# Optimization experiments

Measured on AMD Instinct MI355X. Metric: run time of the kernel, lower is better.

## Reference

```python
import jax, jax.numpy as jnp
import numpy as np

H = 300          # dim_hidden
L = 5            # num_layer
ATOM_VOCAB = 119
BOND_VOCAB = 5

def _bn(h, g, b):
    # train-mode BatchNorm1d over the leading (node/graph) dim
    m = h.mean(axis=0)
    v = h.var(axis=0)
    return g * (h - m) * jax.lax.rsqrt(v + 1e-5) + b

def setup_inputs() -> dict:
    key = jax.random.key(0)
    ks = jax.random.split(key, 24)
    N, E, B = 100000, 200000, 4096
    s = 0.02
    inp = {
        "x": jax.random.randint(ks[0], (N,), 0, ATOM_VOCAB),
        "edge_index": jax.random.randint(ks[1], (2, E), 0, N),
        "edge_attr": jax.random.randint(ks[2], (E,), 0, BOND_VOCAB),
        "batch": jnp.sort(jax.random.randint(ks[3], (N,), 0, B)),
        "batch_size": B,
        "atom_emb": jax.random.normal(ks[4], (ATOM_VOCAB, H)) * s,
        "bond_emb": jax.random.normal(ks[5], (BOND_VOCAB, H)) * s,
        "vn_emb": jax.random.normal(ks[6], (1, H)) * s,
        # per-layer GINE MLP: Linear(H,2H) -> ReLU -> Linear(2H,H), then BN
        "W1": jax.random.normal(ks[7], (L, H, 2 * H)) * s,
        "b1": jnp.zeros((L, 2 * H)),
        "W2": jax.random.normal(ks[8], (L, 2 * H, H)) * s,
        "b2": jnp.zeros((L, H)),
        "bn_g": jnp.ones((L, H)),
        "bn_b": jnp.zeros((L, H)),
        # virtual-node MLP: Lin(H,2H)-BN-ReLU-Lin(2H,H)-BN-ReLU
        "vW1": jax.random.normal(ks[9], (H, 2 * H)) * s,
        "vb1": jnp.zeros((2 * H,)),
        "vg1": jnp.ones((2 * H,)),
        "vbb1": jnp.zeros((2 * H,)),
        "vW2": jax.random.normal(ks[10], (2 * H, H)) * s,
        "vb2": jnp.zeros((H,)),
        "vg2": jnp.ones((H,)),
        "vbb2": jnp.zeros((H,)),
    }
    return inp

def reference(x, edge_index, edge_attr, batch, batch_size,
              atom_emb, bond_emb, vn_emb,
              W1, b1, W2, b2, bn_g, bn_b,
              vW1, vb1, vg1, vbb1, vW2, vb2, vg2, vbb2):
    N = x.shape[0]
    src, dst = edge_index[0], edge_index[1]
    h = atom_emb[x]                       # atom_encoder  [N,H]
    edge_feat = bond_emb[edge_attr]       # bond_encoder  [E,H]
    vn = jnp.broadcast_to(vn_emb[0], (batch_size, H))  # virtual node feats [B,H]
    for i in range(L):
        h_in = h + vn[batch]                                   # broadcast virtual node
        msg = jax.nn.relu(h_in[src] + edge_feat)               # GINE message  [E,H]
        aggr = jax.ops.segment_sum(msg, dst, num_segments=N)   # scatter-add
        pre = h_in + aggr                                      # eps = 0
        out = jax.nn.relu(pre @ W1[i] + b1[i]) @ W2[i] + b2[i]
        out = _bn(out, bn_g[i], bn_b[i])
        if i < L - 1:
            h = jax.nn.relu(out)
            pooled = jax.ops.segment_sum(h, batch, num_segments=batch_size) + vn
            t = jax.nn.relu(_bn(pooled @ vW1 + vb1, vg1, vbb1))
            vn = jax.nn.relu(_bn(t @ vW2 + vb2, vg2, vbb2))
        else:
            h = out                                            # no ReLU on last layer
    # readout: global add pool over graphs
    return jax.ops.segment_sum(h, batch, num_segments=batch_size)  # [B,H]
```

## Files before the change

### kernel.cpp

```cpp
#include <hip/hip_runtime.h>
#include <hip/hip_bf16.h>


#define HD 300
#define HD2 600
#define HDP 304
#define NLAYER 5
#define KS1 10
#define KS2 19
#define CT1P 40
#define CT2P 20
#define CAP 8
#define OVF_MAX 8192

typedef __attribute__((ext_vector_type(8))) short short8v;
typedef __attribute__((ext_vector_type(4))) short short4v;
typedef __attribute__((ext_vector_type(4))) float f32x4;

__device__ __forceinline__ short f2bf(float x) {
  union { float f; unsigned u; } v; v.f = x;
  unsigned r = v.u + 0x7fffu + ((v.u >> 16) & 1u);
  return (short)(r >> 16);
}
__device__ __forceinline__ float bf2f(short h) {
  union { unsigned u; float f; } v; v.u = ((unsigned)(unsigned short)h) << 16;
  return v.f;
}

__device__ __forceinline__ void cvt8(f32x4 x0, f32x4 x1, short8v& fh, short8v& fl) {
#pragma unroll
  for (int j = 0; j < 4; ++j) { short hi = f2bf(x0[j]); fh[j] = hi; fl[j] = f2bf(x0[j] - bf2f(hi)); }
#pragma unroll
  for (int j = 0; j < 4; ++j) { short hi = f2bf(x1[j]); fh[4 + j] = hi; fl[4 + j] = f2bf(x1[j] - bf2f(hi)); }
}

__global__ __launch_bounds__(256) void k_prep_wf(const float* __restrict__ W,
                                                 short* __restrict__ Whi,
                                                 short* __restrict__ Wlo,
                                                 int K, int C, int nks, int total) {
  int idx = blockIdx.x * 256 + threadIdx.x;
  if (idx >= total) return;
  int j = idx & 7, lane = (idx >> 3) & 63, t = idx >> 9;
  int ks = t % nks, ct = t / nks;
  int k = ks * 32 + (lane >> 4) * 8 + j;
  int c = ct * 16 + (lane & 15);
  float w = (k < K && c < C) ? W[(size_t)k * C + c] : 0.f;
  short hi = f2bf(w);
  Whi[idx] = hi;
  Wlo[idx] = f2bf(w - bf2f(hi));
}

__global__ __launch_bounds__(256, 3) void k_mlp_mfma(
    const unsigned short* __restrict__ ph, const unsigned short* __restrict__ pl,
    const short* __restrict__ W1hi, const short* __restrict__ W1lo,
    const float* __restrict__ b1,
    const short* __restrict__ W2hi, const short* __restrict__ W2lo,
    const float* __restrict__ b2, float* __restrict__ out,
    float* __restrict__ stats, int N) {
  __shared__ __align__(16) short hidh[32 * 320];
  __shared__ __align__(16) short hidl[32 * 320];
  char* hbh = (char*)hidh;
  char* hbl = (char*)hidl;
  const int tid = threadIdx.x;
  const int lane = tid & 63, cq = tid >> 6;
  const int li = lane & 15, g = lane >> 4;
  const int row0 = blockIdx.x * 32;
  const size_t r0b = (size_t)(row0 + li) * HDP;
  const size_t r1b = (size_t)(row0 + 16 + li) * HDP;

  f32x4 acc2[2][5];
#pragma unroll
  for (int rt = 0; rt < 2; ++rt)
#pragma unroll
    for (int t = 0; t < 5; ++t) acc2[rt][t] = (f32x4){0.f, 0.f, 0.f, 0.f};

#pragma unroll 1
  for (int hf = 0; hf < 2; ++hf) {
    const int ct0 = hf * 20 + cq * 5;
    f32x4 acc1[2][5];
#pragma unroll
    for (int rt = 0; rt < 2; ++rt)
#pragma unroll
      for (int t = 0; t < 5; ++t) acc1[rt][t] = (f32x4){0.f, 0.f, 0.f, 0.f};
    for (int ks = 0; ks < KS1; ++ks) {
      int k0 = ks * 32 + g * 8;
      short8v a0h = *(const short8v*)(ph + r0b + k0);
      short8v a0l = *(const short8v*)(pl + r0b + k0);
      short8v a1h = *(const short8v*)(ph + r1b + k0);
      short8v a1l = *(const short8v*)(pl + r1b + k0);
      const short8v* whp = (const short8v*)W1hi + ((size_t)ct0 * KS1 + ks) * 64 + lane;
      const short8v* wlp = (const short8v*)W1lo + ((size_t)ct0 * KS1 + ks) * 64 + lane;
#pragma unroll
      for (int ct = 0; ct < 5; ++ct) {
        short8v wh = whp[(size_t)ct * KS1 * 64];
        short8v wl = wlp[(size_t)ct * KS1 * 64];
        acc1[0][ct] = __builtin_amdgcn_mfma_f32_16x16x32_bf16(wh, a0h, acc1[0][ct], 0, 0, 0);
        acc1[0][ct] = __builtin_amdgcn_mfma_f32_16x16x32_bf16(wh, a0l, acc1[0][ct], 0, 0, 0);
        acc1[0][ct] = __builtin_amdgcn_mfma_f32_16x16x32_bf16(wl, a0h, acc1[0][ct], 0, 0, 0);
        acc1[1][ct] = __builtin_amdgcn_mfma_f32_16x16x32_bf16(wh, a1h, acc1[1][ct], 0, 0, 0);
        acc1[1][ct] = __builtin_amdgcn_mfma_f32_16x16x32_bf16(wh, a1l, acc1[1][ct], 0, 0, 0);
        acc1[1][ct] = __builtin_amdgcn_mfma_f32_16x16x32_bf16(wl, a1h, acc1[1][ct], 0, 0, 0);
      }
    }
    if (hf) __syncthreads();
#pragma unroll
    for (int ct = 0; ct < 5; ++ct) {
      int ctile = ct0 + ct, cc = ctile - hf * 20;
      float bb[4];
#pragma unroll
      for (int q = 0; q < 4; ++q) {
        int c = ctile * 16 + g * 4 + q;
        bb[q] = (c < HD2) ? b1[c] : 0.f;
      }
#pragma unroll
      for (int rt = 0; rt < 2; ++rt) {
        short4v vh, vl;
#pragma unroll
        for (int q = 0; q < 4; ++q) {
          float v = fmaxf(acc1[rt][ct][q] + bb[q], 0.f);
          short hi = f2bf(v);
          vh[q] = hi;
          vl[q] = f2bf(v - bf2f(hi));
        }
        int row = rt * 16 + li;
        int lin = row * 640 + cc * 32 + g * 8;
        int sw = (row & 7) << 4;
        *(short4v*)(hbh + (lin ^ sw)) = vh;
        *(short4v*)(hbl + (lin ^ sw)) = vl;
      }
    }
    __syncthreads();
    const int nks2 = hf ? 9 : 10;
    for (int ksl = 0; ksl < nks2; ++ksl) {
      int ksg = hf * 10 + ksl;
      int lin0 = li * 640 + ksl * 64 + g * 16;
      int sw0 = (li & 7) << 4;
      int lin1 = (16 + li) * 640 + ksl * 64 + g * 16;
      int sw1 = ((16 + li) & 7) << 4;
      short8v hh0 = *(const short8v*)(hbh + (lin0 ^ sw0));
      short8v hl0 = *(const short8v*)(hbl + (lin0 ^ sw0));
      short8v hh1 = *(const short8v*)(hbh + (lin1 ^ sw1));
      short8v hl1 = *(const short8v*)(hbl + (lin1 ^ sw1));
      const short8v* w2h = (const short8v*)W2hi + ((size_t)(cq * 5) * KS2 + ksg) * 64 + lane;
      const short8v* w2l = (const short8v*)W2lo + ((size_t)(cq * 5) * KS2 + ksg) * 64 + lane;
#pragma unroll
      for (int t = 0; t < 5; ++t) {
        short8v wh = w2h[(size_t)t * KS2 * 64];
        short8v wl = w2l[(size_t)t * KS2 * 64];
        acc2[0][t] = __builtin_amdgcn_mfma_f32_16x16x32_bf16(hh0, wh, acc2[0][t], 0, 0, 0);
        acc2[0][t] = __builtin_amdgcn_mfma_f32_16x16x32_bf16(hl0, wh, acc2[0][t], 0, 0, 0);
        acc2[0][t] = __builtin_amdgcn_mfma_f32_16x16x32_bf16(hh0, wl, acc2[0][t], 0, 0, 0);
        acc2[1][t] = __builtin_amdgcn_mfma_f32_16x16x32_bf16(hh1, wh, acc2[1][t], 0, 0, 0);
        acc2[1][t] = __builtin_amdgcn_mfma_f32_16x16x32_bf16(hl1, wh, acc2[1][t], 0, 0, 0);
        acc2[1][t] = __builtin_amdgcn_mfma_f32_16x16x32_bf16(hh1, wl, acc2[1][t], 0, 0, 0);
      }
    }
  }
#pragma unroll
  for (int t = 0; t < 5; ++t) {
    int c2 = (cq * 5 + t) * 16 + li;
    if (c2 < HD) {
      float bb = b2[c2];
      float s = 0.f, sq = 0.f;
#pragma unroll
      for (int rt = 0; rt < 2; ++rt) {
#pragma unroll
        for (int q = 0; q < 4; ++q) {
          int gr = row0 + rt * 16 + g * 4 + q;
          if (gr < N) {
            float val = acc2[rt][t][q] + bb;
            out[(size_t)gr * HD + c2] = val;
            s += val;
            sq += val * val;
          }
        }
      }
      s += __shfl_xor(s, 16);  s += __shfl_xor(s, 32);
      sq += __shfl_xor(sq, 16); sq += __shfl_xor(sq, 32);
      if (g == 0) {
        unsafeAtomicAdd(&stats[c2], s);
        unsafeAtomicAdd(&stats[HD + c2], sq);
      }
    }
  }
}

template <int NKS, int NCTQ, bool BNIN, bool STATS>
__global__ __launch_bounds__(512, 2) void k_gemm_mfma(
    const float* __restrict__ A, const float* __restrict__ A2,
    const float* __restrict__ bnst, const float* __restrict__ bng,
    const float* __restrict__ bnb, float invM,
    const short* __restrict__ Whi, const short* __restrict__ Wlo,
    const float* __restrict__ bias, float* __restrict__ outp,
    float* __restrict__ stats_out, int M, int K, int C) {
  const int tid = threadIdx.x, lane = tid & 63, w = tid >> 6;
  const int rtile = w & 1, cq = w >> 1;
  const int li = lane & 15, g = lane >> 4;
  const int row0 = blockIdx.x * 32;
  const int ct0 = cq * NCTQ;
  const int grow = row0 + rtile * 16 + li;
  const float* arow = A + (size_t)grow * K;
  const float* arow2 = A2 ? A2 + (size_t)grow * K : nullptr;
  f32x4 acc[NCTQ];
#pragma unroll
  for (int t = 0; t < NCTQ; ++t) acc[t] = (f32x4){0.f, 0.f, 0.f, 0.f};
  for (int ks = 0; ks < NKS; ++ks) {
    int k0 = ks * 32 + g * 8;
    short8v fh, fl;
    if (grow < M && k0 + 7 < K) {
      f32x4 q0 = *(const f32x4*)(arow + k0);
      f32x4 q1 = *(const f32x4*)(arow + k0 + 4);
      if (arow2) {
        f32x4 u0 = *(const f32x4*)(arow2 + k0);
        f32x4 u1 = *(const f32x4*)(arow2 + k0 + 4);
#pragma unroll
        for (int j = 0; j < 4; ++j) { q0[j] += u0[j]; q1[j] += u1[j]; }
      }
      if (BNIN) {
        f32x4 s0 = *(const f32x4*)(bnst + k0);
        f32x4 s1 = *(const f32x4*)(bnst + k0 + 4);
        f32x4 q20 = *(const f32x4*)(bnst + K + k0);
        f32x4 q21 = *(const f32x4*)(bnst + K + k0 + 4);
        f32x4 g0 = *(const f32x4*)(bng + k0);
        f32x4 g1 = *(const f32x4*)(bng + k0 + 4);
        f32x4 b0 = *(const f32x4*)(bnb + k0);
        f32x4 b1v = *(const f32x4*)(bnb + k0 + 4);
#pragma unroll
        for (int j = 0; j < 4; ++j) {
          float m = s0[j] * invM, vv = q20[j] * invM - m * m;
          q0[j] = fmaxf(g0[j] * (q0[j] - m) * rsqrtf(vv + 1e-5f) + b0[j], 0.f);
          m = s1[j] * invM; vv = q21[j] * invM - m * m;
          q1[j] = fmaxf(g1[j] * (q1[j] - m) * rsqrtf(vv + 1e-5f) + b1v[j], 0.f);
        }
      }
      cvt8(q0, q1, fh, fl);
    } else {
#pragma unroll
      for (int j = 0; j < 8; ++j) {
        int k = k0 + j;
        float v = 0.f;
        if (grow < M && k < K) {
          v = arow[k];
          if (arow2) v += arow2[k];
          if (BNIN) {
            float m = bnst[k] * invM, vv = bnst[K + k] * invM - m * m;
            v = fmaxf(bng[k] * (v - m) * rsqrtf(vv + 1e-5f) + bnb[k], 0.f);
          }
        }
        short hi = f2bf(v); fh[j] = hi; fl[j] = f2bf(v - bf2f(hi));
      }
    }
    const short8v* whp = (const short8v*)Whi + ((size_t)ct0 * NKS + ks) * 64 + lane;
    const short8v* wlp = (const short8v*)Wlo + ((size_t)ct0 * NKS + ks) * 64 + lane;
#pragma unroll
    for (int t = 0; t < NCTQ; ++t) {
      short8v wh = whp[(size_t)t * NKS * 64];
      short8v wl = wlp[(size_t)t * NKS * 64];
      acc[t] = __builtin_amdgcn_mfma_f32_16x16x32_bf16(fh, wh, acc[t], 0, 0, 0);
      acc[t] = __builtin_amdgcn_mfma_f32_16x16x32_bf16(fl, wh, acc[t], 0, 0, 0);
      acc[t] = __builtin_amdgcn_mfma_f32_16x16x32_bf16(fh, wl, acc[t], 0, 0, 0);
    }
  }
#pragma unroll
  for (int t = 0; t < NCTQ; ++t) {
    int c = (ct0 + t) * 16 + li;
    if (c < C) {
      float bb = bias[c];
      float s = 0.f, sq = 0.f;
#pragma unroll
      for (int q = 0; q < 4; ++q) {
        int gr = row0 + rtile * 16 + g * 4 + q;
        if (gr < M) {
          float val = acc[t][q] + bb;
          outp[(size_t)gr * C + c] = val;
          s += val;
          sq += val * val;
        }
      }
      if (STATS) {
        s += __shfl_xor(s, 16);  s += __shfl_xor(s, 32);
        sq += __shfl_xor(sq, 16); sq += __shfl_xor(sq, 32);
        if (g == 0) {
          unsafeAtomicAdd(&stats_out[c], s);
          unsafeAtomicAdd(&stats_out[C + c], sq);
        }
      }
    }
  }
}

__global__ __launch_bounds__(256) void k_scatter(const int* __restrict__ dst,
                                                 int* __restrict__ cnt,
                                                 int* __restrict__ bucket,
                                                 int* __restrict__ ovf,
                                                 int* __restrict__ ovf_cnt, int E) {
  int e = blockIdx.x * 256 + threadIdx.x;
  if (e >= E) return;
  int d = dst[e];
  int pos = atomicAdd(&cnt[d], 1);
  if (pos < CAP) bucket[d * CAP + pos] = e;
  else {
    int p2 = atomicAdd(ovf_cnt, 1);
    if (p2 < OVF_MAX) ovf[p2] = e;
  }
}

__global__ __launch_bounds__(256) void k_bounds(const int* __restrict__ batch,
                                                int* __restrict__ start, int N, int B) {
  int n = blockIdx.x * 256 + threadIdx.x;
  if (n >= N) return;
  int b = batch[n];
  int bp = (n == 0) ? -1 : batch[n - 1];
  for (int g = bp + 1; g <= b; ++g) start[g] = n;
  if (n == N - 1)
    for (int g = b + 1; g <= B; ++g) start[g] = N;
}

__global__ __launch_bounds__(256) void k_aggr(const float* __restrict__ h,
                                              const float* __restrict__ vn,
                                              const float* __restrict__ bond,
                                              const int* __restrict__ batch,
                                              const int* __restrict__ src,
                                              const int* __restrict__ dst,
                                              const int* __restrict__ ea,
                                              const int* __restrict__ bucket,
                                              const int* __restrict__ cnt,
                                              const int* __restrict__ ovf,
                                              const int* __restrict__ ovfc,
                                              unsigned short* __restrict__ ph,
                                              unsigned short* __restrict__ pl, int N) {
  int n = (blockIdx.x * 256 + threadIdx.x) >> 6;
  int lane = threadIdx.x & 63;
  if (n >= N) return;
  int bn = batch[n];
  const float* hn = h + (size_t)n * HD;
  const float* vp = vn + (size_t)bn * HD;
  float acc[5];
#pragma unroll
  for (int j = 0; j < 5; ++j) {
    int col = lane + j * 64;
    acc[j] = (col < HD) ? hn[col] + vp[col] : 0.f;
  }
  int c = cnt[n];
  int cb = min(c, CAP);
  for (int i = 0; i < cb; ++i) {
    int e = bucket[n * CAP + i];
    int s = src[e], a = ea[e], bs = batch[s];
    const float* hs = h + (size_t)s * HD;
    const float* vs = vn + (size_t)bs * HD;
    const float* bb = bond + (size_t)a * HD;
#pragma unroll
    for (int j = 0; j < 5; ++j) {
      int col = lane + j * 64;
      if (col < HD) acc[j] += fmaxf(hs[col] + vs[col] + bb[col], 0.f);
    }
  }
  if (c > CAP) {
    int nov = min(*ovfc, OVF_MAX);
    for (int i = 0; i < nov; ++i) {
      int e = ovf[i];
      if (dst[e] != n) continue;
      int s = src[e], a = ea[e], bs = batch[s];
      const float* hs = h + (size_t)s * HD;
      const float* vs = vn + (size_t)bs * HD;
      const float* bb = bond + (size_t)a * HD;
#pragma unroll
      for (int j = 0; j < 5; ++j) {
        int col = lane + j * 64;
        if (col < HD) acc[j] += fmaxf(hs[col] + vs[col] + bb[col], 0.f);
      }
    }
  }
  unsigned short* phr = ph + (size_t)n * HDP;
  unsigned short* plr = pl + (size_t)n * HDP;
#pragma unroll
  for (int j = 0; j < 5; ++j) {
    int col = lane + j * 64;
    if (col < HDP) {
      float v = (col < HD) ? acc[j] : 0.f;
      short hi = f2bf(v);
      phr[col] = (unsigned short)hi;
      plr[col] = (unsigned short)f2bf(v - bf2f(hi));
    }
  }
}

__global__ __launch_bounds__(64) void k_bn_pool(const float* __restrict__ x,
                                                const float* __restrict__ gw,
                                                const float* __restrict__ bw,
                                                const float* __restrict__ stats,
                                                float invM,
                                                const int* __restrict__ start,
                                                int relu, float* __restrict__ hout,
                                                float* __restrict__ pooled) {
  int grf = blockIdx.x, lane = threadIdx.x;
  int r0 = start[grf], r1 = start[grf + 1];
  float m[5], rs[5], gg[5], bb[5], acc[5];
#pragma unroll
  for (int j = 0; j < 5; ++j) {
    int col = lane + j * 64;
    acc[j] = 0.f;
    m[j] = 0.f; rs[j] = 0.f; gg[j] = 0.f; bb[j] = 0.f;
    if (col < HD) {
      float mm = stats[col] * invM;
      float vv = stats[HD + col] * invM - mm * mm;
      m[j] = mm; rs[j] = rsqrtf(vv + 1e-5f);
      gg[j] = gw[col]; bb[j] = bw[col];
    }
  }
  for (int r = r0; r < r1; ++r) {
    const float* xr = x + (size_t)r * HD;
    float* hr = hout ? hout + (size_t)r * HD : nullptr;
#pragma unroll
    for (int j = 0; j < 5; ++j) {
      int col = lane + j * 64;
      if (col < HD) {
        float val = gg[j] * (xr[col] - m[j]) * rs[j] + bb[j];
        if (relu) val = fmaxf(val, 0.f);
        if (hr) hr[col] = val;
        acc[j] += val;
      }
    }
  }
  float* op = pooled + (size_t)grf * HD;
#pragma unroll
  for (int j = 0; j < 5; ++j) {
    int col = lane + j * 64;
    if (col < HD) op[col] = acc[j];
  }
}

__global__ __launch_bounds__(256) void k_bn_apply(const float* __restrict__ x,
                                                  const float* __restrict__ g,
                                                  const float* __restrict__ b,
                                                  const float* __restrict__ stats,
                                                  float invM, int C, int total, int relu,
                                                  float* __restrict__ out) {
  int idx = blockIdx.x * 256 + threadIdx.x;
  if (idx >= total) return;
  int n = idx / C, c = idx - n * C;
  float m = stats[c] * invM;
  float v = stats[C + c] * invM - m * m;
  float val = g[c] * (x[idx] - m) * rsqrtf(v + 1e-5f) + b[c];
  if (relu) val = fmaxf(val, 0.f);
  out[idx] = val;
}

__global__ __launch_bounds__(256) void k_init_h(const int* __restrict__ x,
                                                const float* __restrict__ emb,
                                                float* __restrict__ h, int nvec) {
  int idx = blockIdx.x * 256 + threadIdx.x;
  if (idx >= nvec) return;
  int n = idx / 75, c4 = idx - n * 75;
  ((float4*)h)[idx] = *(const float4*)(emb + (size_t)x[n] * HD + c4 * 4);
}

__global__ __launch_bounds__(256) void k_init_vn(const float* __restrict__ vn_emb,
                                                 float* __restrict__ vn, int total) {
  int idx = blockIdx.x * 256 + threadIdx.x;
  if (idx >= total) return;
  vn[idx] = vn_emb[idx % HD];
}

extern "C" void kernel_launch(void* const* d_in, const int* in_sizes, int n_in,
                              void* d_out, int out_size, void* d_ws, size_t ws_size,
                              hipStream_t stream) {
  const int N = in_sizes[0];
  const int E = in_sizes[2];
  const int B = out_size / HD;

  const int* x     = (const int*)d_in[0];
  const int* src   = (const int*)d_in[1];
  const int* dst   = src + E;
  const int* ea    = (const int*)d_in[2];
  const int* batch = (const int*)d_in[3];
  const float* atom_emb = (const float*)d_in[5];
  const float* bond_emb = (const float*)d_in[6];
  const float* vn_emb   = (const float*)d_in[7];
  const float* W1   = (const float*)d_in[8];
  const float* b1   = (const float*)d_in[9];
  const float* W2   = (const float*)d_in[10];
  const float* b2   = (const float*)d_in[11];
  const float* bn_g = (const float*)d_in[12];
  const float* bn_b = (const float*)d_in[13];
  const float* vW1  = (const float*)d_in[14];
  const float* vb1  = (const float*)d_in[15];
  const float* vg1  = (const float*)d_in[16];
  const float* vbb1 = (const float*)d_in[17];
  const float* vW2  = (const float*)d_in[18];
  const float* vb2  = (const float*)d_in[19];
  const float* vg2  = (const float*)d_in[20];
  const float* vbb2 = (const float*)d_in[21];

  const size_t NH = (size_t)N * HD;
  const size_t BH = (size_t)B * HD;
  const size_t T1 = (size_t)CT1P * KS1 * 512;
  const size_t T2 = (size_t)CT2P * KS2 * 512;
  const size_t NPAD = (size_t)N + 64;

  char* base = (char*)d_ws;
  size_t off = 0;
  float* h     = (float*)(base + off); off += NH * 4;
  unsigned short* ph = (unsigned short*)(base + off); off += NPAD * HDP * 2;
  unsigned short* pl = (unsigned short*)(base + off); off += NPAD * HDP * 2;
  float* vn    = (float*)(base + off); off += BH * 4;
  float* vt1   = (float*)(base + off); off += (size_t)B * HD2 * 4;
  float* pool  = (float*)(base + off); off += BH * 4;
  float* vt2   = pool;
  float* stats = (float*)(base + off); off += 12000 * 4;
  int* cnt     = (int*)(base + off); off += (size_t)N * 4;
  int* ovfc    = (int*)(base + off); off += 4;
  int* ovf     = (int*)(base + off); off += (size_t)OVF_MAX * 4;
  int* start   = (int*)(base + off); off += (size_t)(B + 1) * 4;
  int* bucket  = (int*)(base + off); off += (size_t)N * CAP * 4;
  off = (off + 15) & ~(size_t)15;
  short* Ahi   = (short*)(base + off); off += T1 * 2;
  short* Alo   = (short*)(base + off); off += T1 * 2;
  short* Bhi   = (short*)(base + off); off += T2 * 2;
  short* Blo   = (short*)(base + off); off += T2 * 2;
  const size_t need_base = off;
  short* vAhi = (short*)(base + off); off += T1 * 2;
  short* vAlo = (short*)(base + off); off += T1 * 2;
  short* vBhi = (short*)(base + off); off += T2 * 2;
  short* vBlo = (short*)(base + off); off += T2 * 2;
  const size_t need_full = off;
  const bool hoist_vw = (ws_size >= need_full);
  if (ws_size < need_base) {
    hipMemsetAsync(d_out, 0, (size_t)out_size * sizeof(float), stream);
    return;
  }
  if (!hoist_vw) { vAhi = Ahi; vAlo = Alo; vBhi = Bhi; vBlo = Blo; }

  hipMemsetAsync(stats, 0, 12000 * sizeof(float) + ((size_t)N + 1) * sizeof(int), stream);

  k_scatter<<<(E + 255) / 256, 256, 0, stream>>>(dst, cnt, bucket, ovf, ovfc, E);
  k_bounds<<<(N + 255) / 256, 256, 0, stream>>>(batch, start, N, B);

  const int totBH = (int)BH;
  const int nvNH = (int)NH / 4;
  const int t1 = (int)T1, t2 = (int)T2;
  k_init_h<<<(nvNH + 255) / 256, 256, 0, stream>>>(x, atom_emb, h, nvNH);
  k_init_vn<<<(totBH + 255) / 256, 256, 0, stream>>>(vn_emb, vn, totBH);
  if (hoist_vw) {
    k_prep_wf<<<(t1 + 255) / 256, 256, 0, stream>>>(vW1, vAhi, vAlo, HD, HD2, KS1, t1);
    k_prep_wf<<<(t2 + 255) / 256, 256, 0, stream>>>(vW2, vBhi, vBlo, HD2, HD, KS2, t2);
  }

  for (int i = 0; i < NLAYER; ++i) {
    float* stL  = stats + i * 2400;
    float* stV1 = stL + 2 * HD;
    float* stV2 = stV1 + 2 * HD2;
    const int last = (i == NLAYER - 1);
    float* pool_i = last ? (float*)d_out : pool;

    k_prep_wf<<<(t1 + 255) / 256, 256, 0, stream>>>(
        W1 + (size_t)i * HD * HD2, Ahi, Alo, HD, HD2, KS1, t1);
    k_prep_wf<<<(t2 + 255) / 256, 256, 0, stream>>>(
        W2 + (size_t)i * HD2 * HD, Bhi, Blo, HD2, HD, KS2, t2);

    k_aggr<<<(N * 64 + 255) / 256, 256, 0, stream>>>(
        h, vn, bond_emb, batch, src, dst, ea, bucket, cnt, ovf, ovfc, ph, pl, N);
    k_mlp_mfma<<<(N + 31) / 32, 256, 0, stream>>>(
        ph, pl, Ahi, Alo, b1 + (size_t)i * HD2, Bhi, Blo, b2 + (size_t)i * HD,
        h, stL, N);
    k_bn_pool<<<B, 64, 0, stream>>>(h, bn_g + i * HD, bn_b + i * HD, stL,
                                    1.f / (float)N, start, last ? 0 : 1,
                                    last ? nullptr : h, pool_i);

    if (!last) {
      if (!hoist_vw) {
        k_prep_wf<<<(t1 + 255) / 256, 256, 0, stream>>>(vW1, vAhi, vAlo, HD, HD2, KS1, t1);
      }
      k_gemm_mfma<KS1, 10, false, true><<<B / 32, 512, 0, stream>>>(
          pool, vn, nullptr, nullptr, nullptr, 0.f, vAhi, vAlo, vb1, vt1, stV1, B, HD, HD2);
      if (!hoist_vw) {
        k_prep_wf<<<(t2 + 255) / 256, 256, 0, stream>>>(vW2, vBhi, vBlo, HD2, HD, KS2, t2);
      }
      k_gemm_mfma<KS2, 5, true, true><<<B / 32, 512, 0, stream>>>(
          vt1, nullptr, stV1, vg1, vbb1, 1.f / (float)B, vBhi, vBlo, vb2, vt2, stV2, B, HD2, HD);
      k_bn_apply<<<(totBH + 255) / 256, 256, 0, stream>>>(
          vt2, vg2, vbb2, stV2, 1.f / (float)B, HD, totBH, 1, vn);
    }
  }
}
```

Before: 3.771 ms.

## Split MLP row tiles across waves with 512-thread blocks

The fused MLP kernel now runs 8 waves per block instead of 4, with each wave handling one 16-row tile rather than both. This halves the accumulator registers per wave and raises the launch-bounds occupancy target, aiming to hide memory and MFMA latency better. In exchange, each weight fragment is loaded from global memory by twice as many waves, so per-wave weight reuse is lower and cache traffic is higher.

```diff
diff --git a/kernel.cpp b/kernel.cpp
--- a/kernel.cpp
+++ b/kernel.cpp
@@ -50,7 +50,7 @@
   Wlo[idx] = f2bf(w - bf2f(hi));
 }
 
-__global__ __launch_bounds__(256, 3) void k_mlp_mfma(
+__global__ __launch_bounds__(512, 4) void k_mlp_mfma(
     const unsigned short* __restrict__ ph, const unsigned short* __restrict__ pl,
     const short* __restrict__ W1hi, const short* __restrict__ W1lo,
     const float* __restrict__ b1,
@@ -62,97 +62,73 @@
   char* hbh = (char*)hidh;
   char* hbl = (char*)hidl;
   const int tid = threadIdx.x;
-  const int lane = tid & 63, cq = tid >> 6;
+  const int lane = tid & 63, w = tid >> 6;
+  const int rt = w & 1, cq = w >> 1;
   const int li = lane & 15, g = lane >> 4;
   const int row0 = blockIdx.x * 32;
-  const size_t r0b = (size_t)(row0 + li) * HDP;
-  const size_t r1b = (size_t)(row0 + 16 + li) * HDP;
-
-  f32x4 acc2[2][5];
-#pragma unroll
-  for (int rt = 0; rt < 2; ++rt)
-#pragma unroll
-    for (int t = 0; t < 5; ++t) acc2[rt][t] = (f32x4){0.f, 0.f, 0.f, 0.f};
+  const int lrow = rt * 16 + li;
+  const size_t rb = (size_t)(row0 + lrow) * HDP;
+  const int sw = (lrow & 7) << 4;
+
+  f32x4 acc2[5];
+#pragma unroll
+  for (int t = 0; t < 5; ++t) acc2[t] = (f32x4){0.f, 0.f, 0.f, 0.f};
 
 #pragma unroll 1
   for (int hf = 0; hf < 2; ++hf) {
     const int ct0 = hf * 20 + cq * 5;
-    f32x4 acc1[2][5];
-#pragma unroll
-    for (int rt = 0; rt < 2; ++rt)
-#pragma unroll
-      for (int t = 0; t < 5; ++t) acc1[rt][t] = (f32x4){0.f, 0.f, 0.f, 0.f};
+    f32x4 acc1[5];
+#pragma unroll
+    for (int t = 0; t < 5; ++t) acc1[t] = (f32x4){0.f, 0.f, 0.f, 0.f};
     for (int ks = 0; ks < KS1; ++ks) {
       int k0 = ks * 32 + g * 8;
-      short8v a0h = *(const short8v*)(ph + r0b + k0);
-      short8v a0l = *(const short8v*)(pl + r0b + k0);
-      short8v a1h = *(const short8v*)(ph + r1b + k0);
-      short8v a1l = *(const short8v*)(pl + r1b + k0);
+      short8v ah = *(const short8v*)(ph + rb + k0);
+      short8v al = *(const short8v*)(pl + rb + k0);
       const short8v* whp = (const short8v*)W1hi + ((size_t)ct0 * KS1 + ks) * 64 + lane;
       const short8v* wlp = (const short8v*)W1lo + ((size_t)ct0 * KS1 + ks) * 64 + lane;
 #pragma unroll
       for (int ct = 0; ct < 5; ++ct) {
         short8v wh = whp[(size_t)ct * KS1 * 64];
         short8v wl = wlp[(size_t)ct * KS1 * 64];
-        acc1[0][ct] = __builtin_amdgcn_mfma_f32_16x16x32_bf16(wh, a0h, acc1[0][ct], 0, 0, 0);
-        acc1[0][ct] = __builtin_amdgcn_mfma_f32_16x16x32_bf16(wh, a0l, acc1[0][ct], 0, 0, 0);
-        acc1[0][ct] = __builtin_amdgcn_mfma_f32_16x16x32_bf16(wl, a0h, acc1[0][ct], 0, 0, 0);
-        acc1[1][ct] = __builtin_amdgcn_mfma_f32_16x16x32_bf16(wh, a1h, acc1[1][ct], 0, 0, 0);
-        acc1[1][ct] = __builtin_amdgcn_mfma_f32_16x16x32_bf16(wh, a1l, acc1[1][ct], 0, 0, 0);
-        acc1[1][ct] = __builtin_amdgcn_mfma_f32_16x16x32_bf16(wl, a1h, acc1[1][ct], 0, 0, 0);
+        acc1[ct] = __builtin_amdgcn_mfma_f32_16x16x32_bf16(wh, ah, acc1[ct], 0, 0, 0);
+        acc1[ct] = __builtin_amdgcn_mfma_f32_16x16x32_bf16(wh, al, acc1[ct], 0, 0, 0);
+        acc1[ct] = __builtin_amdgcn_mfma_f32_16x16x32_bf16(wl, ah, acc1[ct], 0, 0, 0);
       }
     }
     if (hf) __syncthreads();
 #pragma unroll
     for (int ct = 0; ct < 5; ++ct) {
       int ctile = ct0 + ct, cc = ctile - hf * 20;
-      float bb[4];
+      short4v vh, vl;
 #pragma unroll
       for (int q = 0; q < 4; ++q) {
         int c = ctile * 16 + g * 4 + q;
-        bb[q] = (c < HD2) ? b1[c] : 0.f;
-      }
-#pragma unroll
-      for (int rt = 0; rt < 2; ++rt) {
-        short4v vh, vl;
-#pragma unroll
-        for (int q = 0; q < 4; ++q) {
-          float v = fmaxf(acc1[rt][ct][q] + bb[q], 0.f);
-          short hi = f2bf(v);
-          vh[q] = hi;
-          vl[q] = f2bf(v - bf2f(hi));
-        }
-        int row = rt * 16 + li;
-        int lin = row * 640 + cc * 32 + g * 8;
-        int sw = (row & 7) << 4;
-        *(short4v*)(hbh + (lin ^ sw)) = vh;
-        *(short4v*)(hbl + (lin ^ sw)) = vl;
-      }
+        float bb = (c < HD2) ? b1[c] : 0.f;
+        float v = fmaxf(acc1[ct][q] + bb, 0.f);
+        short hi = f2bf(v);
+        vh[q] = hi;
+        vl[q] = f2bf(v - bf2f(hi));
+      }
+      int lin = lrow * 640 + cc * 32 + g * 8;
+      *(short4v*)(hbh + (lin ^ sw)) = vh;
+      *(short4v*)(hbl + (lin ^ sw)) = vl;
     }
     __syncthreads();
     const int nks2 = hf ? 9 : 10;
     for (int ksl = 0; ksl < nks2; ++ksl) {
       int ksg = hf * 10 + ksl;
-      int lin0 = li * 640 + ksl * 64 + g * 16;
-      int sw0 = (li & 7) << 4;
-      int lin1 = (16 + li) * 640 + ksl * 64 + g * 16;
-      int sw1 = ((16 + li) & 7) << 4;
-      short8v hh0 = *(const short8v*)(hbh + (lin0 ^ sw0));
-      short8v hl0 = *(const short8v*)(hbl + (lin0 ^ sw0));
-      short8v hh1 = *(const short8v*)(hbh + (lin1 ^ sw1));
-      short8v hl1 = *(const short8v*)(hbl + (lin1 ^ sw1));
+      int lin = lrow * 640 + ksl * 64 + g * 16;
+      short8v hh = *(const short8v*)(hbh + (lin ^ sw));
+      short8v hl = *(const short8v*)(hbl + (lin ^ sw));
       const short8v* w2h = (const short8v*)W2hi + ((size_t)(cq * 5) * KS2 + ksg) * 64 + lane;
       const short8v* w2l = (const short8v*)W2lo + ((size_t)(cq * 5) * KS2 + ksg) * 64 + lane;
 #pragma unroll
       for (int t = 0; t < 5; ++t) {
         short8v wh = w2h[(size_t)t * KS2 * 64];
         short8v wl = w2l[(size_t)t * KS2 * 64];
-        acc2[0][t] = __builtin_amdgcn_mfma_f32_16x16x32_bf16(hh0, wh, acc2[0][t], 0, 0, 0);
-        acc2[0][t] = __builtin_amdgcn_mfma_f32_16x16x32_bf16(hl0, wh, acc2[0][t], 0, 0, 0);
-        acc2[0][t] = __builtin_amdgcn_mfma_f32_16x16x32_bf16(hh0, wl, acc2[0][t], 0, 0, 0);
-        acc2[1][t] = __builtin_amdgcn_mfma_f32_16x16x32_bf16(hh1, wh, acc2[1][t], 0, 0, 0);
-        acc2[1][t] = __builtin_amdgcn_mfma_f32_16x16x32_bf16(hl1, wh, acc2[1][t], 0, 0, 0);
-        acc2[1][t] = __builtin_amdgcn_mfma_f32_16x16x32_bf16(hh1, wl, acc2[1][t], 0, 0, 0);
+        acc2[t] = __builtin_amdgcn_mfma_f32_16x16x32_bf16(hh, wh, acc2[t], 0, 0, 0);
+        acc2[t] = __builtin_amdgcn_mfma_f32_16x16x32_bf16(hl, wh, acc2[t], 0, 0, 0);
+        acc2[t] = __builtin_amdgcn_mfma_f32_16x16x32_bf16(hh, wl, acc2[t], 0, 0, 0);
       }
     }
   }
@@ -163,16 +139,13 @@
       float bb = b2[c2];
       float s = 0.f, sq = 0.f;
 #pragma unroll
-      for (int rt = 0; rt < 2; ++rt) {
-#pragma unroll
-        for (int q = 0; q < 4; ++q) {
-          int gr = row0 + rt * 16 + g * 4 + q;
-          if (gr < N) {
-            float val = acc2[rt][t][q] + bb;
-            out[(size_t)gr * HD + c2] = val;
-            s += val;
-            sq += val * val;
-          }
+      for (int q = 0; q < 4; ++q) {
+        int gr = row0 + rt * 16 + g * 4 + q;
+        if (gr < N) {
+          float val = acc2[t][q] + bb;
+          out[(size_t)gr * HD + c2] = val;
+          s += val;
+          sq += val * val;
         }
       }
       s += __shfl_xor(s, 16);  s += __shfl_xor(s, 32);
@@ -560,7 +533,7 @@
 
     k_aggr<<<(N * 64 + 255) / 256, 256, 0, stream>>>(
         h, vn, bond_emb, batch, src, dst, ea, bucket, cnt, ovf, ovfc, ph, pl, N);
-    k_mlp_mfma<<<(N + 31) / 32, 256, 0, stream>>>(
+    k_mlp_mfma<<<(N + 31) / 32, 512, 0, stream>>>(
         ph, pl, Ahi, Alo, b1 + (size_t)i * HD2, Bhi, Blo, b2 + (size_t)i * HD,
         h, stL, N);
     k_bn_pool<<<B, 64, 0, stream>>>(h, bn_g + i * HD, bn_b + i * HD, stL,
```

New measurement: 6.177 ms. +63.8%, slower.
